# Performance work log

Hardware: AMD Instinct MI355X
Metric: run time of the kernel (lower is better)

Reference implementation:

```python
import jax, jax.numpy as jnp
import numpy as np

B = 128          # batch of IQ signals
L = 128          # signal length
PL = 16          # patch length
ST = 4           # patch stride
WIN = 4          # local window
NPATCH = (L - PL) // ST + 1   # 29
HID = 256
NCLS = 8
NG = B * NPATCH               # number of patch graphs
N = NG * PL                   # total nodes


def _build_edges():
    src, dst = [], []
    for i in range(PL):
        for j in range(PL):
            if 0 < abs(i - j) <= WIN:
                src.append(i); dst.append(j)
    bs = np.array(src, np.int32)          # [108]
    bd = np.array(dst, np.int32)
    off = (np.arange(NG, dtype=np.int32) * PL)[:, None]
    isrc = (off + bs[None, :]).reshape(-1)
    idst = (off + bd[None, :]).reshape(-1)
    # cross-patch edges: last node of patch p -> first node of patch p+1
    b = np.arange(B, dtype=np.int32)[:, None]
    p = np.arange(NPATCH - 1, dtype=np.int32)[None, :]
    csrc = (b * NPATCH * PL + p * PL + (PL - 1)).reshape(-1)
    cdst = (b * NPATCH * PL + (p + 1) * PL).reshape(-1)
    return np.concatenate([isrc, csrc]), np.concatenate([idst, cdst])


def setup_inputs() -> dict:
    key = jax.random.key(0)
    ks = jax.random.split(key, 10)
    s = 0.05
    esrc, edst = _build_edges()
    return {
        "iq_signal": jax.random.normal(ks[0], (B, 2, L), jnp.float32),
        "edge_src": jnp.asarray(esrc),
        "edge_dst": jnp.asarray(edst),
        # SAGEConv layer 0 (in=2): lin_l (agg, with bias), lin_r (root, no bias)
        "W0_agg": jax.random.normal(ks[1], (HID, 2), jnp.float32) * s,
        "W0_root": jax.random.normal(ks[2], (HID, 2), jnp.float32) * s,
        "b0": jnp.zeros((HID,), jnp.float32),
        # SAGEConv layers 1..3 (256 -> 256), stacked
        "W_agg": jax.random.normal(ks[3], (3, HID, HID), jnp.float32) * s,
        "W_root": jax.random.normal(ks[4], (3, HID, HID), jnp.float32) * s,
        "b_lin": jnp.zeros((3, HID), jnp.float32),
        # per-layer LayerNorms
        "ln_scale": jnp.ones((4, HID), jnp.float32),
        "ln_bias": jnp.zeros((4, HID), jnp.float32),
        # classifier head
        "cls_W1": jax.random.normal(ks[5], (HID, HID), jnp.float32) * s,
        "cls_b1": jnp.zeros((HID,), jnp.float32),
        "cls_ln_scale": jnp.ones((HID,), jnp.float32),
        "cls_ln_bias": jnp.zeros((HID,), jnp.float32),
        "cls_W2": jax.random.normal(ks[6], (NCLS, HID), jnp.float32) * s,
        "cls_b2": jnp.zeros((NCLS,), jnp.float32),
    }


def _ln(x, g, b):
    m = x.mean(-1, keepdims=True)
    v = ((x - m) ** 2).mean(-1, keepdims=True)
    return (x - m) * jax.lax.rsqrt(v + 1e-5) * g + b


def reference(iq_signal, edge_src, edge_dst, W0_agg, W0_root, b0,
              W_agg, W_root, b_lin, ln_scale, ln_bias,
              cls_W1, cls_b1, cls_ln_scale, cls_ln_bias, cls_W2, cls_b2):
    # patch extraction: [B,2,L] -> [B,NPATCH,PL,2] -> node features [N,2]
    idx = jnp.arange(NPATCH)[:, None] * ST + jnp.arange(PL)[None, :]   # [29,16]
    x = jnp.transpose(iq_signal[:, :, idx], (0, 2, 3, 1)).reshape(-1, 2)

    # in-degree for mean aggregation (0 -> safe divide by 1)
    ones = jnp.ones((edge_dst.shape[0],), x.dtype)
    deg = jax.ops.segment_sum(ones, edge_dst, num_segments=N)
    inv_deg = 1.0 / jnp.maximum(deg, 1.0)

    def sage(h, Wa, Wr, b):
        # mean-aggregate neighbor messages, then lin_l(agg) + lin_r(h) + bias
        agg = jax.ops.segment_sum(h[edge_src], edge_dst, num_segments=N)
        agg = agg * inv_deg[:, None]
        return agg @ Wa.T + h @ Wr.T + b

    # layer 0 (2 -> 256): no residual (shape change)
    h = jax.nn.relu(_ln(sage(x, W0_agg, W0_root, b0), ln_scale[0], ln_bias[0]))
    # layers 1..3 with residual
    for l in range(3):
        hn = jax.nn.relu(_ln(sage(h, W_agg[l], W_root[l], b_lin[l]),
                             ln_scale[l + 1], ln_bias[l + 1]))
        h = h + hn

    node_emb = h                                  # [N, 256]
    # global_mean_pool per patch graph (16 consecutive nodes each)
    gf = node_emb.reshape(NG, PL, HID).mean(axis=1)   # [NG, 256]
    z = jax.nn.relu(_ln(gf @ cls_W1.T + cls_b1, cls_ln_scale, cls_ln_bias))
    logits = z @ cls_W2.T + cls_b2                # [NG, 8]
    return logits, gf, node_emb
```

## Files before the change

### kernel.cpp

```cpp
#include <hip/hip_runtime.h>
#include <hip/hip_bf16.h>

typedef __hip_bfloat16 bf16;
typedef unsigned short u16;
typedef unsigned int uint32;
typedef __attribute__((ext_vector_type(8))) short bf16x8;
typedef __attribute__((ext_vector_type(4))) float f32x4;

#define BATCH   128
#define LSIG    128
#define PL      16
#define ST      4
#define WIN     4
#define NPATCH  29
#define NG      (BATCH * NPATCH)
#define NNODE   (NG * PL)
#define HID     256
#define NCLS    8

#define IQ_OFF    0
#define W0A_OFF   32768
#define W0R_OFF   33280
#define B0_OFF    33792
#define BLIN_OFF  34048
#define LNS_OFF   34816
#define LNB_OFF   35840
#define W1T_OFF   36864
#define CB1_OFF   102400
#define CLNS_OFF  102656
#define CLNB_OFF  102912
#define CW2_OFF   103168
#define CB2_OFF   105216
#define CVT_TOTAL 105224
#define WB_TOTAL  393216

#define P_BYTE_OFF   4096
#define WB_BYTE_OFF  425984
#define A_BYTE_OFF   1216512
#define B_BYTE_OFF   1959936
#define GF_EOFF      (NG * NCLS)
#define EMB_EOFF     (NG * NCLS + NG * HID)

#define MFMA_BF16 __builtin_amdgcn_mfma_f32_16x16x32_bf16

__device__ __forceinline__ float b2f(bf16 x) { return __bfloat162float(x); }
__device__ __forceinline__ float lof(uint32 u) { return __uint_as_float(u << 16); }
__device__ __forceinline__ float hif(uint32 u) { return __uint_as_float(u & 0xFFFF0000u); }
__device__ __forceinline__ uint32 packbf(float a, float b) {
  bf16 r0 = __float2bfloat16(a), r1 = __float2bfloat16(b);
  return ((uint32)(*(const u16*)&r1) << 16) | (uint32)(*(const u16*)&r0);
}
__device__ __forceinline__ float ldmix(const void* p, size_t i, int fl) {
  return fl ? ((const float*)p)[i] : __bfloat162float(((const bf16*)p)[i]);
}

__global__ __launch_bounds__(256) void detect_kernel(const u16* __restrict__ iq, int* flag) {
  __shared__ int sbig, snz;
  int t = threadIdx.x;
  if (t == 0) { sbig = 0; snz = 0; }
  __syncthreads();
  int big = 0, nz = 0;
  for (int e = t; e < 16384; e += 256) {
    u16 u = iq[2 * e];
    int ex = (u >> 7) & 0xFF;
    if (ex >= 0xC0) big++;
    if (u != 0) nz++;
  }
  atomicAdd(&sbig, big); atomicAdd(&snz, nz);
  __syncthreads();
  if (t == 0) *flag = (sbig > 4 || snz < 100) ? 1 : 0;
}

__global__ __launch_bounds__(256) void convert_all(
    const int* __restrict__ flag,
    const void* iq, const void* w0a, const void* w0r, const void* b0,
    const void* blin, const void* lns, const void* lnb,
    const void* cw1, const void* cb1, const void* clns, const void* clnb,
    const void* cw2, const void* cb2,
    const void* wag, const void* wro,
    float* __restrict__ P, bf16* __restrict__ WB) {
  int idx = blockIdx.x * 256 + threadIdx.x;
  int fl = *flag;
  if (idx < CVT_TOTAL) {
    float v;
    if (idx < W0A_OFF)        v = ldmix(iq,  idx, fl);
    else if (idx < W0R_OFF)   v = ldmix(w0a, idx - W0A_OFF, fl);
    else if (idx < B0_OFF)    v = ldmix(w0r, idx - W0R_OFF, fl);
    else if (idx < BLIN_OFF)  v = ldmix(b0,  idx - B0_OFF, fl);
    else if (idx < LNS_OFF)   v = ldmix(blin, idx - BLIN_OFF, fl);
    else if (idx < LNB_OFF)   v = ldmix(lns, idx - LNS_OFF, fl);
    else if (idx < W1T_OFF)   v = ldmix(lnb, idx - LNB_OFF, fl);
    else if (idx < CB1_OFF) { int t2 = idx - W1T_OFF;
      v = ldmix(cw1, (t2 & 255) * 256 + (t2 >> 8), fl); }
    else if (idx < CLNS_OFF)  v = ldmix(cb1, idx - CB1_OFF, fl);
    else if (idx < CLNB_OFF)  v = ldmix(clns, idx - CLNS_OFF, fl);
    else if (idx < CW2_OFF)   v = ldmix(clnb, idx - CLNB_OFF, fl);
    else if (idx < CB2_OFF)   v = ldmix(cw2, idx - CW2_OFF, fl);
    else                      v = ldmix(cb2, idx - CB2_OFF, fl);
    P[idx] = v;
  } else if (idx < CVT_TOTAL + WB_TOTAL) {
    int k = idx - CVT_TOTAL;
    int l = k >> 17, m = (k >> 16) & 1, r = k & 65535;
    const void* src = m ? wro : wag;
    WB[k] = __float2bfloat16(ldmix(src, l * 65536 + r, fl));
  }
}

__global__ __launch_bounds__(256) void layer0_kernel(
    const float* __restrict__ P, bf16* __restrict__ hout) {
  int g = blockIdx.x, f = threadIdx.x;
  int b = g / NPATCH, p = g % NPATCH;
  __shared__ float x_s[PL][2];
  __shared__ float xp_s[2];
  __shared__ float agg_s[PL][2];
  __shared__ float o_s[PL][HID];
  __shared__ float mv_s[PL][2];
  if (f < 32) { int j = f & 15, c = f >> 4;
    x_s[j][c] = P[IQ_OFF + (b * 2 + c) * LSIG + p * ST + j]; }
  if (f < 2) xp_s[f] = (p > 0) ? P[IQ_OFF + (b * 2 + f) * LSIG + (p - 1) * ST + PL - 1] : 0.f;
  __syncthreads();
  if (f < 32) { int j = f & 15, c = f >> 4;
    float s = 0.f;
    int lo = j - WIN < 0 ? 0 : j - WIN, hi = j + WIN > 15 ? 15 : j + WIN;
    for (int i = lo; i <= hi; ++i) if (i != j) s += x_s[i][c];
    int deg = (j < WIN ? j : WIN) + ((15 - j) < WIN ? (15 - j) : WIN);
    if (j == 0 && p > 0) { s += xp_s[c]; deg += 1; }
    agg_s[j][c] = s / (float)deg;
  }
  __syncthreads();
  float wa0 = P[W0A_OFF + f * 2], wa1 = P[W0A_OFF + f * 2 + 1];
  float wr0 = P[W0R_OFF + f * 2], wr1 = P[W0R_OFF + f * 2 + 1];
  float bb = P[B0_OFF + f];
#pragma unroll
  for (int j = 0; j < PL; ++j)
    o_s[j][f] = agg_s[j][0] * wa0 + agg_s[j][1] * wa1 + x_s[j][0] * wr0 + x_s[j][1] * wr1 + bb;
  __syncthreads();
  { int j = f >> 4, q = f & 15;
    float s = 0.f, s2 = 0.f;
#pragma unroll
    for (int i = 0; i < 16; ++i) { float v = o_s[j][q + 16 * i]; s += v; s2 += v * v; }
#pragma unroll
    for (int m = 8; m >= 1; m >>= 1) { s += __shfl_xor(s, m); s2 += __shfl_xor(s2, m); }
    if (q == 0) { float mean = s * (1.f / HID);
      float var = s2 * (1.f / HID) - mean * mean;
      mv_s[j][0] = mean; mv_s[j][1] = rsqrtf(var + 1e-5f); }
  }
  __syncthreads();
  float gl = P[LNS_OFF + f], bl = P[LNB_OFF + f];
#pragma unroll
  for (int j = 0; j < PL; ++j) {
    float v = (o_s[j][f] - mv_s[j][0]) * mv_s[j][1] * gl + bl;
    v = v > 0.f ? v : 0.f;
    hout[(size_t)(g * PL + j) * HID + f] = __float2bfloat16(v);
  }
}

template<int LAST>
__global__ __launch_bounds__(256, 2) void sage_mfma(
    const bf16* __restrict__ hin,
    const bf16* __restrict__ Wa, const bf16* __restrict__ Wr,
    const float* __restrict__ bias,
    const float* __restrict__ lng, const float* __restrict__ lnb,
    bf16* __restrict__ hout,
    void* __restrict__ dout, const int* __restrict__ flag) {
  int t = threadIdx.x;
  int w = t >> 6, l = t & 63, lr = l & 15, lg = l >> 4;
  int g0 = blockIdx.x * 4;
  size_t nbase = (size_t)g0 * PL;
  __shared__ uint32 h32[64 * 128];
  __shared__ uint32 a32[64 * 128];
  float* mvp = (float*)h32;
  const uint32* hinw = (const uint32*)hin;

  int colbase = w * 64;
  const bf16* waB = Wa + (colbase + lr) * HID + lg * 8;
  const bf16* wrB = Wr + (colbase + lr) * HID + lg * 8;
  bf16x8 wa0[2][8], wr0[2][8];
#pragma unroll
  for (int nt = 0; nt < 2; ++nt)
#pragma unroll
    for (int ks = 0; ks < 8; ++ks) {
      wa0[nt][ks] = *(const bf16x8*)(waB + nt * 16 * HID + ks * 32);
      wr0[nt][ks] = *(const bf16x8*)(wrB + nt * 16 * HID + ks * 32);
    }

  const uint32* hg = hinw + nbase * 128;
#pragma unroll
  for (int it = 0; it < 8; ++it) {
    int u = it * 256 + t;
    int row = u >> 5, sl = u & 31;
    int sw = sl ^ (row & 7);
    *(uint4*)&h32[row * 128 + sw * 4] = *(const uint4*)(hg + u * 4);
  }
  __syncthreads();

  {
    int c2 = t & 127, Ph = t >> 7;
#pragma unroll
    for (int pi = 0; pi < 2; ++pi) {
      int pp = Ph + pi * 2;
      int pr = pp * 16;
      int hp = ((g0 + pp) % NPATCH) != 0;
      float vlo[16], vhi[16];
#pragma unroll
      for (int j = 0; j < 16; ++j) {
        uint32 u = h32[(pr + j) * 128 + (((c2 >> 2) ^ (j & 7)) << 2) + (c2 & 3)];
        vlo[j] = lof(u); vhi[j] = hif(u);
      }
      float blo = 0.f, bhi = 0.f;
      if (hp) {
        uint32 u;
        if (pp == 0) u = hinw[(nbase - 1) * 128 + c2];
        else { int br = pr - 1;
          u = h32[br * 128 + (((c2 >> 2) ^ (br & 7)) << 2) + (c2 & 3)]; }
        blo = lof(u); bhi = hif(u);
      }
#pragma unroll
      for (int j = 0; j < 16; ++j) {
        const int a = (j - WIN < 0) ? 0 : j - WIN;
        const int b = (j + WIN > 15) ? 15 : j + WIN;
        float slo = 0.f, shi = 0.f;
#pragma unroll
        for (int i = 0; i < 16; ++i)
          if (i >= a && i <= b && i != j) { slo += vlo[i]; shi += vhi[i]; }
        float deg = (float)((j < WIN ? j : WIN) + (15 - j < WIN ? 15 - j : WIN));
        if (j == 0 && hp) { slo += blo; shi += bhi; deg += 1.f; }
        float inv = 1.f / deg;
        a32[(pr + j) * 128 + (((c2 >> 2) ^ (j & 7)) << 2) + (c2 & 3)] = packbf(slo * inv, shi * inv);
      }
    }
  }
  __syncthreads();

  f32x4 acc[4][4];
#pragma unroll
  for (int m = 0; m < 4; ++m)
#pragma unroll
    for (int n = 0; n < 4; ++n) acc[m][n] = (f32x4){0.f, 0.f, 0.f, 0.f};
#pragma unroll
  for (int ks = 0; ks < 8; ++ks) {
    bf16x8 wa1[2], wr1[2];
#pragma unroll
    for (int nt = 0; nt < 2; ++nt) {
      wa1[nt] = *(const bf16x8*)(waB + (nt + 2) * 16 * HID + ks * 32);
      wr1[nt] = *(const bf16x8*)(wrB + (nt + 2) * 16 * HID + ks * 32);
    }
#pragma unroll
    for (int m = 0; m < 4; ++m) {
      int idx = (m * 16 + lr) * 128 + (((ks * 4 + lg) ^ (lr & 7)) << 2);
      bf16x8 af = *(const bf16x8*)&a32[idx];
      bf16x8 hf = *(const bf16x8*)&h32[idx];
      acc[m][0] = MFMA_BF16(af, wa0[0][ks], acc[m][0], 0, 0, 0);
      acc[m][0] = MFMA_BF16(hf, wr0[0][ks], acc[m][0], 0, 0, 0);
      acc[m][1] = MFMA_BF16(af, wa0[1][ks], acc[m][1], 0, 0, 0);
      acc[m][1] = MFMA_BF16(hf, wr0[1][ks], acc[m][1], 0, 0, 0);
      acc[m][2] = MFMA_BF16(af, wa1[0],     acc[m][2], 0, 0, 0);
      acc[m][2] = MFMA_BF16(hf, wr1[0],     acc[m][2], 0, 0, 0);
      acc[m][3] = MFMA_BF16(af, wa1[1],     acc[m][3], 0, 0, 0);
      acc[m][3] = MFMA_BF16(hf, wr1[1],     acc[m][3], 0, 0, 0);
    }
  }
#pragma unroll
  for (int nt = 0; nt < 4; ++nt) {
    float bv = bias[colbase + nt * 16 + lr];
#pragma unroll
    for (int m = 0; m < 4; ++m) {
      acc[m][nt][0] += bv; acc[m][nt][1] += bv; acc[m][nt][2] += bv; acc[m][nt][3] += bv;
    }
  }
  __syncthreads();

#pragma unroll
  for (int m = 0; m < 4; ++m)
#pragma unroll
    for (int nt = 0; nt < 4; ++nt) {
      int col = colbase + nt * 16 + lr;
#pragma unroll
      for (int r = 0; r < 4; ++r) {
        int row = m * 16 + lg * 4 + r;
        int i16 = row * 256 + (((col >> 3) ^ (row & 7)) << 3) + (col & 7);
        bf16 x = __float2bfloat16(acc[m][nt][r]);
        ((u16*)a32)[i16] = *(const u16*)&x;
      }
    }
  __syncthreads();

  {
    int row = t >> 2, q = t & 3;
    float s = 0.f, s2 = 0.f;
#pragma unroll
    for (int i = 0; i < 32; ++i) {
      int d = q * 32 + i;
      uint32 u = a32[row * 128 + (((d >> 2) ^ (row & 7)) << 2) + (d & 3)];
      float a = lof(u), b = hif(u);
      s += a + b; s2 += a * a + b * b;
    }
    s += __shfl_xor(s, 1); s2 += __shfl_xor(s2, 1);
    s += __shfl_xor(s, 2); s2 += __shfl_xor(s2, 2);
    if (q == 0) { float mean = s * (1.f / HID);
      mvp[row * 2] = mean;
      mvp[row * 2 + 1] = rsqrtf(s2 * (1.f / HID) - mean * mean + 1e-5f); }
  }
  __syncthreads();

  {
    int c2 = t & 127, prt = t >> 7;
    float gl0 = lng[c2 * 2], gl1 = lng[c2 * 2 + 1];
    float bl0 = lnb[c2 * 2], bl1 = lnb[c2 * 2 + 1];
    uint32* outw = nullptr;
    if constexpr (!LAST) outw = (uint32*)hout + nbase * 128;
    const uint32* inw = hinw + nbase * 128;
    int fl = 0;
    if constexpr (LAST) fl = *flag;
#pragma unroll
    for (int pi = 0; pi < 2; ++pi) {
      float sga = 0.f, sgb = 0.f;
#pragma unroll
      for (int i = 0; i < 16; ++i) {
        int row = prt * 32 + pi * 16 + i;
        uint32 u = a32[row * 128 + (((c2 >> 2) ^ (row & 7)) << 2) + (c2 & 3)];
        float mean = mvp[row * 2], rstd = mvp[row * 2 + 1];
        float a = (lof(u) - mean) * rstd * gl0 + bl0; a = a > 0.f ? a : 0.f;
        float b_ = (hif(u) - mean) * rstd * gl1 + bl1; b_ = b_ > 0.f ? b_ : 0.f;
        uint32 hu = inw[row * 128 + c2];
        a += lof(hu); b_ += hif(hu);
        if constexpr (!LAST) {
          outw[row * 128 + c2] = packbf(a, b_);
        } else {
          sga += a; sgb += b_;
          if (fl) {
            size_t ei = (size_t)EMB_EOFF + (nbase + row) * 256 + (size_t)c2 * 2;
            *(float2*)&((float*)dout)[ei] = make_float2(a, b_);
          } else {
            ((uint32*)dout)[(EMB_EOFF >> 1) + (nbase + row) * 128 + c2] = packbf(a, b_);
          }
        }
      }
      if constexpr (LAST) {
        float ga = sga * (1.f / PL), gb = sgb * (1.f / PL);
        int gidx = g0 + prt * 2 + pi;
        if (fl) {
          size_t gi = (size_t)GF_EOFF + (size_t)gidx * 256 + (size_t)c2 * 2;
          *(float2*)&((float*)dout)[gi] = make_float2(ga, gb);
        } else {
          ((uint32*)dout)[(GF_EOFF >> 1) + gidx * 128 + c2] = packbf(ga, gb);
        }
      }
    }
  }
}

__global__ __launch_bounds__(256) void head_kernel(
    const void* __restrict__ gin, const float* __restrict__ P,
    void* __restrict__ dout, const int* __restrict__ flag) {
  int g = blockIdx.x, f = threadIdx.x;
  int fl = *flag;
  __shared__ float gf_s[HID];
  __shared__ float z_s[HID];
  __shared__ float ps[4], ps2[4];
  __shared__ float mr[2];
  gf_s[f] = fl ? ((const float*)gin)[(size_t)GF_EOFF + (size_t)g * HID + f]
               : b2f(((const bf16*)gin)[(size_t)GF_EOFF + (size_t)g * HID + f]);
  __syncthreads();
  float acc = P[CB1_OFF + f];
  for (int k = 0; k < HID; k += 4) {
    const float4 gv = *(const float4*)(&gf_s[k]);
    acc = fmaf(gv.x, P[W1T_OFF + (k + 0) * HID + f], acc);
    acc = fmaf(gv.y, P[W1T_OFF + (k + 1) * HID + f], acc);
    acc = fmaf(gv.z, P[W1T_OFF + (k + 2) * HID + f], acc);
    acc = fmaf(gv.w, P[W1T_OFF + (k + 3) * HID + f], acc);
  }
  float s1 = acc, s2 = acc * acc;
#pragma unroll
  for (int m = 32; m >= 1; m >>= 1) { s1 += __shfl_xor(s1, m); s2 += __shfl_xor(s2, m); }
  int wid = f >> 6, lane = f & 63;
  if (lane == 0) { ps[wid] = s1; ps2[wid] = s2; }
  __syncthreads();
  if (f == 0) {
    float S = ps[0] + ps[1] + ps[2] + ps[3];
    float S2 = ps2[0] + ps2[1] + ps2[2] + ps2[3];
    float mean = S * (1.f / HID);
    mr[0] = mean; mr[1] = rsqrtf(S2 * (1.f / HID) - mean * mean + 1e-5f);
  }
  __syncthreads();
  float z = (acc - mr[0]) * mr[1] * P[CLNS_OFF + f] + P[CLNB_OFF + f];
  z = z > 0.f ? z : 0.f;
  z_s[f] = z;
  __syncthreads();
  {
    int cls = f >> 5, lane = f & 31;
    float a = 0.f;
    for (int k = lane; k < HID; k += 32)
      a = fmaf(z_s[k], P[CW2_OFF + cls * HID + k], a);
    a += __shfl_xor(a, 16); a += __shfl_xor(a, 8);
    a += __shfl_xor(a, 4);  a += __shfl_xor(a, 2); a += __shfl_xor(a, 1);
    if (lane == 0) {
      a += P[CB2_OFF + cls];
      size_t ei = (size_t)g * NCLS + cls;
      if (fl) ((float*)dout)[ei] = a; else ((bf16*)dout)[ei] = __float2bfloat16(a);
    }
  }
}

extern "C" void kernel_launch(void* const* d_in, const int* in_sizes, int n_in,
                              void* d_out, int out_size, void* d_ws, size_t ws_size,
                              hipStream_t stream) {
  char* ws = (char*)d_ws;
  int*   flag = (int*)ws;
  float* P    = (float*)(ws + P_BYTE_OFF);
  bf16*  WB   = (bf16*)(ws + WB_BYTE_OFF);
  bf16*  A    = (bf16*)(ws + A_BYTE_OFF);
  bf16*  B    = (bf16*)((char*)d_out + B_BYTE_OFF);

  detect_kernel<<<1, 256, 0, stream>>>((const u16*)d_in[0], flag);
  convert_all<<<(CVT_TOTAL + WB_TOTAL + 255) / 256, 256, 0, stream>>>(
      flag, d_in[0], d_in[3], d_in[4], d_in[5], d_in[8],
      d_in[9], d_in[10], d_in[11], d_in[12], d_in[13], d_in[14], d_in[15], d_in[16],
      d_in[6], d_in[7], P, WB);

  layer0_kernel<<<NG, 256, 0, stream>>>(P, A);
  sage_mfma<0><<<NG / 4, 256, 0, stream>>>(A, WB, WB + 65536,
      P + BLIN_OFF, P + LNS_OFF + HID, P + LNB_OFF + HID, B, nullptr, flag);
  sage_mfma<0><<<NG / 4, 256, 0, stream>>>(B, WB + 131072, WB + 131072 + 65536,
      P + BLIN_OFF + HID, P + LNS_OFF + 2 * HID, P + LNB_OFF + 2 * HID, A, nullptr, flag);
  sage_mfma<1><<<NG / 4, 256, 0, stream>>>(A, WB + 262144, WB + 262144 + 65536,
      P + BLIN_OFF + 2 * HID, P + LNS_OFF + 3 * HID, P + LNB_OFF + 3 * HID, nullptr, d_out, flag);
  head_kernel<<<NG, 256, 0, stream>>>(d_out, P, d_out, flag);
}
```

Measured before the change: 231.1 us.

## Store hidden states pre-swizzled and load them straight into LDS

Layer outputs are now written to global memory already in the XOR-swizzled order that the shared-memory tiles use. Each SAGE layer can then fill its LDS tile with global_load_lds, which copies without passing data through registers or recomputing the swizzle per element. All readers of the intermediate buffer (the cross-patch neighbour row, the residual read and the output write) switch to the swizzled index. The final embedding output keeps the natural layout. The MFMA loop is also wrapped in s_setprio to give its waves scheduling priority. The risk is that the global accesses are now permuted within each row, which may change coalescing.

```diff
diff --git a/kernel.cpp b/kernel.cpp
--- a/kernel.cpp
+++ b/kernel.cpp
@@ -52,6 +52,11 @@
 }
 __device__ __forceinline__ float ldmix(const void* p, size_t i, int fl) {
   return fl ? ((const float*)p)[i] : __bfloat162float(((const bf16*)p)[i]);
+}
+__device__ __forceinline__ void gl_lds16(const uint32* gsrc, uint32* ldst) {
+  __builtin_amdgcn_global_load_lds(
+      (const __attribute__((address_space(1))) uint32*)gsrc,
+      (__attribute__((address_space(3))) uint32*)ldst, 16, 0, 0);
 }
 
 __global__ __launch_bounds__(256) void detect_kernel(const u16* __restrict__ iq, int* flag) {
@@ -151,7 +156,8 @@
   for (int j = 0; j < PL; ++j) {
     float v = (o_s[j][f] - mv_s[j][0]) * mv_s[j][1] * gl + bl;
     v = v > 0.f ? v : 0.f;
-    hout[(size_t)(g * PL + j) * HID + f] = __float2bfloat16(v);
+    bf16 x = __float2bfloat16(v);
+    ((u16*)hout)[(size_t)(g * PL + j) * 256 + ((((f >> 3) ^ (j & 7))) << 3) + (f & 7)] = *(const u16*)&x;
   }
 }
 
@@ -184,13 +190,11 @@
       wr0[nt][ks] = *(const bf16x8*)(wrB + nt * 16 * HID + ks * 32);
     }
 
-  const uint32* hg = hinw + nbase * 128;
+  const uint32* hgw = hinw + nbase * 128;
 #pragma unroll
   for (int it = 0; it < 8; ++it) {
-    int u = it * 256 + t;
-    int row = u >> 5, sl = u & 31;
-    int sw = sl ^ (row & 7);
-    *(uint4*)&h32[row * 128 + sw * 4] = *(const uint4*)(hg + u * 4);
+    int off = (it * 4 + w) * 256;
+    gl_lds16(hgw + off + (l << 2), &h32[off]);
   }
   __syncthreads();
 
@@ -210,7 +214,7 @@
       float blo = 0.f, bhi = 0.f;
       if (hp) {
         uint32 u;
-        if (pp == 0) u = hinw[(nbase - 1) * 128 + c2];
+        if (pp == 0) u = hinw[(nbase - 1) * 128 + (((c2 >> 2) ^ 7) << 2) + (c2 & 3)];
         else { int br = pr - 1;
           u = h32[br * 128 + (((c2 >> 2) ^ (br & 7)) << 2) + (c2 & 3)]; }
         blo = lof(u); bhi = hif(u);
@@ -237,6 +241,7 @@
   for (int m = 0; m < 4; ++m)
 #pragma unroll
     for (int n = 0; n < 4; ++n) acc[m][n] = (f32x4){0.f, 0.f, 0.f, 0.f};
+  __builtin_amdgcn_s_setprio(1);
 #pragma unroll
   for (int ks = 0; ks < 8; ++ks) {
     bf16x8 wa1[2], wr1[2];
@@ -260,6 +265,7 @@
       acc[m][3] = MFMA_BF16(hf, wr1[1],     acc[m][3], 0, 0, 0);
     }
   }
+  __builtin_amdgcn_s_setprio(0);
 #pragma unroll
   for (int nt = 0; nt < 4; ++nt) {
     float bv = bias[colbase + nt * 16 + lr];
@@ -318,14 +324,15 @@
 #pragma unroll
       for (int i = 0; i < 16; ++i) {
         int row = prt * 32 + pi * 16 + i;
-        uint32 u = a32[row * 128 + (((c2 >> 2) ^ (row & 7)) << 2) + (c2 & 3)];
+        int pidx = row * 128 + (((c2 >> 2) ^ (row & 7)) << 2) + (c2 & 3);
+        uint32 u = a32[pidx];
         float mean = mvp[row * 2], rstd = mvp[row * 2 + 1];
         float a = (lof(u) - mean) * rstd * gl0 + bl0; a = a > 0.f ? a : 0.f;
         float b_ = (hif(u) - mean) * rstd * gl1 + bl1; b_ = b_ > 0.f ? b_ : 0.f;
-        uint32 hu = inw[row * 128 + c2];
+        uint32 hu = inw[pidx];
         a += lof(hu); b_ += hif(hu);
         if constexpr (!LAST) {
-          outw[row * 128 + c2] = packbf(a, b_);
+          outw[pidx] = packbf(a, b_);
         } else {
           sga += a; sgb += b_;
           if (fl) {
@@ -388,13 +395,13 @@
   z_s[f] = z;
   __syncthreads();
   {
-    int cls = f >> 5, lane = f & 31;
+    int cls = f >> 5, lane2 = f & 31;
     float a = 0.f;
-    for (int k = lane; k < HID; k += 32)
+    for (int k = lane2; k < HID; k += 32)
       a = fmaf(z_s[k], P[CW2_OFF + cls * HID + k], a);
     a += __shfl_xor(a, 16); a += __shfl_xor(a, 8);
     a += __shfl_xor(a, 4);  a += __shfl_xor(a, 2); a += __shfl_xor(a, 1);
-    if (lane == 0) {
+    if (lane2 == 0) {
       a += P[CB2_OFF + cls];
       size_t ei = (size_t)g * NCLS + cls;
       if (fl) ((float*)dout)[ei] = a; else ((bf16*)dout)[ei] = __float2bfloat16(a);
```

New measurement: 225.3 us, median of 2. -2.5%, faster.
